# Kernel optimization log

Hardware: AMD Instinct MI355X
Metric: run time of the kernel (lower is better)

## Reference

```python
import jax, jax.numpy as jnp
import numpy as np

N, E, T, CIN, COUT = 20000, 160000, 8, 64, 128


def setup_inputs() -> dict:
    key = jax.random.key(0)
    ks = jax.random.split(key, 8)
    x = jax.random.normal(ks[0], (T, N, CIN), jnp.float32)
    edge_index = jax.random.randint(ks[1], (2, E), 0, N)
    edge_weight = jax.random.normal(ks[2], (E,), jnp.float32)
    # temporal Conv1d: kernel 3, xavier-ish small init (gain=0.1 in source)
    tconv_w = jax.random.normal(ks[3], (COUT, CIN, 3), jnp.float32) * 0.02
    tconv_b = jnp.zeros((COUT,), jnp.float32)
    ln_g = jnp.ones((COUT,), jnp.float32)
    ln_b = jnp.zeros((COUT,), jnp.float32)
    # residual 1x1 Conv1d (in != out channels)
    res_w = jax.random.normal(ks[4], (COUT, CIN), jnp.float32) * 0.05
    res_b = jnp.zeros((COUT,), jnp.float32)
    # GCNConv linear weight [out, in] and bias
    gcn_w = jax.random.normal(ks[5], (COUT, COUT), jnp.float32) * 0.05
    gcn_b = jnp.zeros((COUT,), jnp.float32)
    return dict(x=x, edge_index=edge_index, edge_weight=edge_weight,
                tconv_w=tconv_w, tconv_b=tconv_b, ln_g=ln_g, ln_b=ln_b,
                res_w=res_w, res_b=res_b, gcn_w=gcn_w, gcn_b=gcn_b)


def reference(x, edge_index, edge_weight, tconv_w, tconv_b, ln_g, ln_b,
              res_w, res_b, gcn_w, gcn_b):
    Tn, Nn, _ = x.shape
    xc = jnp.transpose(x, (1, 2, 0))  # [N, Cin, T]
    # temporal conv over T (kernel 3, pad 1)
    h = jax.lax.conv_general_dilated(
        xc, tconv_w, window_strides=(1,), padding=[(1, 1)],
        dimension_numbers=('NCH', 'OIH', 'NCH')) + tconv_b[None, :, None]
    h = jnp.transpose(h, (0, 2, 1))  # [N, T, Cout]
    # LayerNorm over channel dim
    mu = h.mean(-1, keepdims=True)
    var = ((h - mu) ** 2).mean(-1, keepdims=True)
    h = (h - mu) * jax.lax.rsqrt(var + 1e-5) * ln_g + ln_b
    h = jax.nn.relu(h)
    # 1x1 residual conv: [N,Cin,T] x [Cout,Cin] -> [N,T,Cout]
    res = jnp.einsum('nct,oc->nto', xc, res_w) + res_b
    xcmb = h + res  # [N, T, Cout]
    # --- GCNConv (PyG): softmax edge weights, self-loops, sym-normalize ---
    ew = jax.nn.softmax(edge_weight)  # softmax over all edges (dim=0)
    row, col = edge_index[0], edge_index[1]
    sl = jnp.arange(Nn)
    row_f = jnp.concatenate([row, sl])
    col_f = jnp.concatenate([col, sl])
    w_f = jnp.concatenate([ew, jnp.ones((Nn,), ew.dtype)])  # self-loop weight 1
    deg = jax.ops.segment_sum(w_f, col_f, num_segments=Nn)
    dinv = jnp.where(deg > 0, jax.lax.rsqrt(jnp.maximum(deg, 1e-12)), 0.0)
    norm = dinv[row_f] * w_f * dinv[col_f]  # [E+N]
    xt = jnp.einsum('ntc,oc->nto', xcmb, gcn_w)  # linear transform, all T at once
    msg = norm[:, None, None] * xt[row_f]        # gather sources: [E+N, T, Cout]
    agg = jax.ops.segment_sum(msg, col_f, num_segments=Nn) + gcn_b
    out = jax.nn.relu(agg)  # [N, T, Cout]
    return jnp.transpose(out, (1, 0, 2))  # [T, N, Cout] == stacked per-t list
```

## Files before the change

### kernel.cpp

```cpp
#include <hip/hip_runtime.h>
#include <math.h>

#define N_NODES 20000
#define E_EDGES 160000
#define T_STEPS 8
#define C_IN    64
#define C_OUT   128

typedef __bf16 bf16x8 __attribute__((ext_vector_type(8)));
typedef float  f32x4  __attribute__((ext_vector_type(4)));
#define MFMA16(a, b, c) __builtin_amdgcn_mfma_f32_16x16x32_bf16((a), (b), (c), 0, 0, 0)

__device__ __forceinline__ unsigned short f2u(float f) {
  __bf16 b = (__bf16)f;
  return __builtin_bit_cast(unsigned short, b);
}
__device__ __forceinline__ unsigned int pack2(float lo, float hi) {
  return (unsigned int)f2u(lo) | ((unsigned int)f2u(hi) << 16);
}

__device__ __forceinline__ float wredSum(float v) {
#pragma unroll
  for (int d = 32; d > 0; d >>= 1) v += __shfl_xor(v, d, 64);
  return v;
}
__device__ __forceinline__ float wredMax(float v) {
#pragma unroll
  for (int d = 32; d > 0; d >>= 1) v = fmaxf(v, __shfl_xor(v, d, 64));
  return v;
}
__device__ __forceinline__ int wredSumI(int v) {
#pragma unroll
  for (int d = 32; d > 0; d >>= 1) v += __shfl_xor(v, d, 64);
  return v;
}
__device__ __forceinline__ float bredSum(float v, float* sm4) {
  __syncthreads();
  v = wredSum(v);
  const int lane = threadIdx.x & 63, wid = threadIdx.x >> 6;
  if (lane == 0) sm4[wid] = v;
  __syncthreads();
  return sm4[0] + sm4[1] + sm4[2] + sm4[3];
}
__device__ __forceinline__ float bredMax(float v, float* sm4) {
  __syncthreads();
  v = wredMax(v);
  const int lane = threadIdx.x & 63, wid = threadIdx.x >> 6;
  if (lane == 0) sm4[wid] = v;
  __syncthreads();
  return fmaxf(fmaxf(sm4[0], sm4[1]), fmaxf(sm4[2], sm4[3]));
}
__device__ __forceinline__ int bredSumI(int v, int* sm4) {
  __syncthreads();
  v = wredSumI(v);
  const int lane = threadIdx.x & 63, wid = threadIdx.x >> 6;
  if (lane == 0) sm4[wid] = v;
  __syncthreads();
  return sm4[0] + sm4[1] + sm4[2] + sm4[3];
}

__global__ __launch_bounds__(256) void k_esoft(const float* __restrict__ w,
                                               float* __restrict__ pm, float* __restrict__ ps) {
  __shared__ float sm4[4];
  float m = -3.4e38f, s = 0.f;
  for (int i = blockIdx.x * 256 + threadIdx.x; i < E_EDGES; i += 256 * 256) {
    const float xw = w[i];
    if (xw > m) { s = s * expf(m - xw) + 1.f; m = xw; }
    else        { s += expf(xw - m); }
  }
  const float M = bredMax(m, sm4);
  const float sp = (s > 0.f) ? s * expf(m - M) : 0.f;
  const float S = bredSum(sp, sm4);
  if (threadIdx.x == 0) { pm[blockIdx.x] = M; ps[blockIdx.x] = S; }
}

__global__ __launch_bounds__(256) void k_edge(const float* __restrict__ w, const int* __restrict__ ei,
                                              const float* __restrict__ pm, const float* __restrict__ ps,
                                              float* __restrict__ ewv, float* __restrict__ deg,
                                              int* __restrict__ cnt) {
  __shared__ float sm4[4];
  const float mloc = pm[threadIdx.x];
  const float mx   = bredMax(mloc, sm4);
  const float sp   = ps[threadIdx.x] * expf(mloc - mx);
  const float sum  = bredSum(sp, sm4);
  const int e = blockIdx.x * 256 + threadIdx.x;
  const float v = expf(w[e] - mx) / sum;
  ewv[e] = v;
  const int c = ei[E_EDGES + e];
  atomicAdd(&deg[c], v);
  atomicAdd(&cnt[c], 1);
}

__global__ __launch_bounds__(256) void k_scanA(const int* __restrict__ cnt, const float* __restrict__ deg,
                                               float* __restrict__ dinv, int* __restrict__ csum) {
  __shared__ int sm4[4];
  const int i = blockIdx.x * 256 + threadIdx.x;
  const int v = (i < N_NODES) ? cnt[i] : 0;
  if (i < N_NODES) dinv[i] = rsqrtf(deg[i]);
  int s = wredSumI(v);
  const int lane = threadIdx.x & 63, wid = threadIdx.x >> 6;
  if (lane == 0) sm4[wid] = s;
  __syncthreads();
  if (threadIdx.x == 0) csum[blockIdx.x] = sm4[0] + sm4[1] + sm4[2] + sm4[3];
}

__global__ __launch_bounds__(256) void k_scanC(const int* __restrict__ cnt, const int* __restrict__ csum,
                                               int* __restrict__ off, int* __restrict__ cursor) {
  __shared__ int smI[4];
  __shared__ int wpart[4];
  const int tid = threadIdx.x, lane = tid & 63, wid = tid >> 6;
  const int nchunk = (N_NODES + 255) / 256;
  const int vb = (tid < nchunk && tid < blockIdx.x) ? csum[tid] : 0;
  const int base = bredSumI(vb, smI);
  const int i = blockIdx.x * 256 + tid;
  const int v = (i < N_NODES) ? cnt[i] : 0;
  int s = v;
#pragma unroll
  for (int d = 1; d < 64; d <<= 1) { const int u = __shfl_up(s, d, 64); if (lane >= d) s += u; }
  if (lane == 63) wpart[wid] = s;
  __syncthreads();
  int add = base;
#pragma unroll
  for (int wv = 0; wv < 4; ++wv) if (wv < wid) add += wpart[wv];
  if (i < N_NODES) { const int excl = add + (s - v); off[i] = excl; cursor[i] = excl; }
  if (i == N_NODES - 1) off[N_NODES] = E_EDGES;
}

__global__ __launch_bounds__(256) void k_norm_scatter(const int* __restrict__ ei, const float* __restrict__ ewv,
                                                      const float* __restrict__ dinv, int* __restrict__ cursor,
                                                      uint2* __restrict__ srcnrm) {
  const int e = blockIdx.x * 256 + threadIdx.x;
  const int r = ei[e], c = ei[E_EDGES + e];
  const float nm = dinv[r] * ewv[e] * dinv[c];
  const int pos = atomicAdd(&cursor[c], 1);
  srcnrm[pos] = make_uint2((unsigned int)r, __builtin_bit_cast(unsigned int, nm));
}

__global__ __launch_bounds__(256) void k_wprep(const float* __restrict__ tconv_w, const float* __restrict__ res_w,
                                               const float* __restrict__ gcn_w, unsigned int* __restrict__ Bf,
                                               float* __restrict__ deg, int* __restrict__ cnt) {
  const int gid = blockIdx.x * 256 + threadIdx.x;
  if (gid < N_NODES) { deg[gid] = 1.0f; cnt[gid] = 0; }
  float v0, v1;
  if (gid < 12288) {
    const int reg = gid & 3, l = (gid >> 2) & 63, ct = (gid >> 8) & 7, ks = gid >> 11;
    const int o = ct * 16 + (l & 15);
    const int k0 = ks * 32 + ((l >> 4) & 3) * 8 + reg * 2;
    const int c0 = k0 & 63, tap0 = k0 >> 6;
    const int c1 = (k0 + 1) & 63, tap1 = (k0 + 1) >> 6;
    v0 = tconv_w[o * 192 + c0 * 3 + tap0];
    v1 = tconv_w[o * 192 + c1 * 3 + tap1];
  } else if (gid < 16384) {
    const int g = gid - 12288;
    const int reg = g & 3, l = (g >> 2) & 63, ct = (g >> 8) & 7, ks = g >> 11;
    const int o = ct * 16 + (l & 15);
    const int k0 = ks * 32 + ((l >> 4) & 3) * 8 + reg * 2;
    v0 = res_w[o * 64 + k0];
    v1 = res_w[o * 64 + k0 + 1];
  } else {
    const int g = gid - 16384;
    const int reg = g & 3, l = (g >> 2) & 63, ct = (g >> 8) & 7, ks = g >> 11;
    const int o = ct * 16 + (l & 15);
    const int k0 = ks * 32 + ((l >> 4) & 3) * 8 + reg * 2;
    v0 = gcn_w[o * 128 + k0];
    v1 = gcn_w[o * 128 + k0 + 1];
  }
  Bf[gid] = pack2(v0, v1);
}

#define XS_NODE 720
#define XS_SLOT 72
#define AS2_STRIDE 136
__global__ __launch_bounds__(256, 2) void k_fuse(const float* __restrict__ x,
                                                 const float* __restrict__ tconv_b,
                                                 const float* __restrict__ ln_g, const float* __restrict__ ln_b,
                                                 const float* __restrict__ res_b,
                                                 const unsigned int* __restrict__ Bf,
                                                 unsigned char* __restrict__ xq,
                                                 float* __restrict__ qsc) {
  const int tid = threadIdx.x, lane = tid & 63, w = tid >> 6;
  const int l15 = lane & 15, lg = lane >> 4;
  const int n0 = blockIdx.x * 16;

  __shared__ __align__(16) unsigned short XsAs[128 * AS2_STRIDE];
  unsigned short* Xs  = XsAs;
  unsigned short* As2 = XsAs;
  __shared__ float psum[4][128], psq[4][128];
  __shared__ float smu[128], srs[128];
  __shared__ float pmax4[4][16];
  __shared__ float smax16[16];

#pragma unroll
  for (int p = 0; p < 8; ++p) {
    const int chunk = p * 256 + tid;
    const int tq = chunk >> 8, nn = (chunk >> 4) & 15, c4 = chunk & 15;
    const float4 v = *(const float4*)(x + ((size_t)tq * N_NODES + n0 + nn) * C_IN + c4 * 4);
    uint2 pk; pk.x = pack2(v.x, v.y); pk.y = pack2(v.z, v.w);
    *(uint2*)&Xs[nn * XS_NODE + (tq + 1) * XS_SLOT + c4 * 4] = pk;
  }
#pragma unroll
  for (int p = 0; p < 3; ++p) {
    const int i = p * 256 + tid;
    if (i < 576) {
      const int nn = i / 36;
      const int r = i - nn * 36;
      const int sl = (r < 18) ? 0 : 9;
      const int of = ((r < 18) ? r : r - 18) * 4;
      *(uint2*)&Xs[nn * XS_NODE + sl * XS_SLOT + of] = make_uint2(0u, 0u);
    }
  }

  const uint4* Bf4 = (const uint4*)Bf;
  uint4 Bc[2][6], Br[2][2];
#pragma unroll
  for (int ct = 0; ct < 2; ++ct) {
    const int ctg = w * 2 + ct;
#pragma unroll
    for (int ks = 0; ks < 6; ++ks) Bc[ct][ks] = Bf4[(ks * 8 + ctg) * 64 + lane];
#pragma unroll
    for (int ks = 0; ks < 2; ++ks) Br[ct][ks] = Bf4[3072 + (ks * 8 + ctg) * 64 + lane];
  }
  float cb[2], rb[2], gv[2], bv[2];
#pragma unroll
  for (int ct = 0; ct < 2; ++ct) {
    const int col = w * 32 + ct * 16 + l15;
    cb[ct] = tconv_b[col]; rb[ct] = res_b[col]; gv[ct] = ln_g[col]; bv[ct] = ln_b[col];
  }
  __syncthreads();

  f32x4 accC[8][2], accR[8][2];
#pragma unroll
  for (int rt = 0; rt < 8; ++rt)
#pragma unroll
    for (int ct = 0; ct < 2; ++ct) { accC[rt][ct] = (f32x4)0.f; accR[rt][ct] = (f32x4)0.f; }

#pragma unroll
  for (int ks = 0; ks < 6; ++ks) {
    bf16x8 af[8];
    const int slot = (l15 & 7) + (ks >> 1);
    const int koff = slot * XS_SLOT + (ks & 1) * 32 + lg * 8;
#pragma unroll
    for (int rt = 0; rt < 8; ++rt) {
      const int node = rt * 2 + (l15 >> 3);
      af[rt] = *(const bf16x8*)&Xs[node * XS_NODE + koff];
    }
#pragma unroll
    for (int rt = 0; rt < 8; ++rt)
#pragma unroll
      for (int ct = 0; ct < 2; ++ct)
        accC[rt][ct] = MFMA16(af[rt], __builtin_bit_cast(bf16x8, Bc[ct][ks]), accC[rt][ct]);
    if (ks == 2 || ks == 3) {
#pragma unroll
      for (int rt = 0; rt < 8; ++rt)
#pragma unroll
        for (int ct = 0; ct < 2; ++ct)
          accR[rt][ct] = MFMA16(af[rt], __builtin_bit_cast(bf16x8, Br[ct][ks - 2]), accR[rt][ct]);
    }
  }

#pragma unroll
  for (int rt = 0; rt < 8; ++rt) {
    float s[4], s2[4];
#pragma unroll
    for (int j = 0; j < 4; ++j) {
      const float h0 = accC[rt][0][j] + cb[0];
      const float h1 = accC[rt][1][j] + cb[1];
      accC[rt][0][j] = h0; accC[rt][1][j] = h1;
      s[j] = h0 + h1; s2[j] = h0 * h0 + h1 * h1;
    }
#pragma unroll
    for (int d = 1; d < 16; d <<= 1)
#pragma unroll
      for (int j = 0; j < 4; ++j) { s[j] += __shfl_xor(s[j], d, 64); s2[j] += __shfl_xor(s2[j], d, 64); }
    if (l15 == 0)
#pragma unroll
      for (int j = 0; j < 4; ++j) {
        psum[w][rt * 16 + lg * 4 + j] = s[j];
        psq[w][rt * 16 + lg * 4 + j] = s2[j];
      }
  }
  __syncthreads();
  if (tid < 128) {
    const float S  = psum[0][tid] + psum[1][tid] + psum[2][tid] + psum[3][tid];
    const float S2 = psq[0][tid] + psq[1][tid] + psq[2][tid] + psq[3][tid];
    const float mu = S * (1.f / 128.f);
    const float var = S2 * (1.f / 128.f) - mu * mu;
    smu[tid] = mu; srs[tid] = rsqrtf(var + 1e-5f);
  }
  __syncthreads();

#pragma unroll
  for (int rt = 0; rt < 8; ++rt)
#pragma unroll
    for (int j = 0; j < 4; ++j) {
      const int row = rt * 16 + lg * 4 + j;
      const float mu = smu[row], rs = srs[row];
      const int sw = ((row >> 3) & 1) << 4;
#pragma unroll
      for (int ct = 0; ct < 2; ++ct) {
        float xc = (accC[rt][ct][j] - mu) * rs * gv[ct] + bv[ct];
        xc = fmaxf(xc, 0.f) + accR[rt][ct][j] + rb[ct];
        const int col = w * 32 + ct * 16 + l15;
        As2[row * AS2_STRIDE + (col ^ sw)] = f2u(xc);
      }
    }
  __syncthreads();

  uint4 Bg[2][4];
#pragma unroll
  for (int ct = 0; ct < 2; ++ct)
#pragma unroll
    for (int ks = 0; ks < 4; ++ks) Bg[ct][ks] = Bf4[4096 + (ks * 8 + (w * 2 + ct)) * 64 + lane];

  f32x4 acc[8][2];
#pragma unroll
  for (int rt = 0; rt < 8; ++rt)
#pragma unroll
    for (int ct = 0; ct < 2; ++ct) acc[rt][ct] = (f32x4)0.f;

  const int swr = ((l15 >> 3) & 1) << 4;
#pragma unroll
  for (int ks = 0; ks < 4; ++ks) {
    bf16x8 af[8];
    const int koff = (ks * 32 + lg * 8) ^ swr;
#pragma unroll
    for (int rt = 0; rt < 8; ++rt)
      af[rt] = *(const bf16x8*)&As2[(rt * 16 + l15) * AS2_STRIDE + koff];
#pragma unroll
    for (int rt = 0; rt < 8; ++rt)
#pragma unroll
      for (int ct = 0; ct < 2; ++ct)
        acc[rt][ct] = MFMA16(af[rt], __builtin_bit_cast(bf16x8, Bg[ct][ks]), acc[rt][ct]);
  }

#pragma unroll
  for (int rt = 0; rt < 8; ++rt) {
    float m = 0.f;
#pragma unroll
    for (int ct = 0; ct < 2; ++ct)
#pragma unroll
      for (int j = 0; j < 4; ++j) m = fmaxf(m, fabsf(acc[rt][ct][j]));
#pragma unroll
    for (int d = 1; d < 32; d <<= 1) m = fmaxf(m, __shfl_xor(m, d, 64));
    if ((lane & 31) == 0) pmax4[w][rt * 2 + (lane >> 5)] = m;
  }
  __syncthreads();
  if (tid < 16) {
    const float mx = fmaxf(fmaxf(pmax4[0][tid], pmax4[1][tid]), fmaxf(pmax4[2][tid], pmax4[3][tid]));
    smax16[tid] = mx;
    qsc[n0 + tid] = mx * (1.f / 127.f);
  }
  __syncthreads();

  const int t0 = (lg & 1) * 4;
#pragma unroll
  for (int rt = 0; rt < 8; ++rt) {
    const int nn = rt * 2 + (lg >> 1);
    const size_t n = (size_t)(n0 + nn);
    const float mx = smax16[nn];
    const float inv = (mx > 0.f) ? 127.f / mx : 0.f;
#pragma unroll
    for (int ct = 0; ct < 2; ++ct) {
      const int col = w * 32 + ct * 16 + l15;
      unsigned int pk8 = 0;
#pragma unroll
      for (int j = 0; j < 4; ++j) {
        const int q = (int)rintf(acc[rt][ct][j] * inv) + 128;
        pk8 |= ((unsigned int)q) << (8 * j);
      }
      *(unsigned int*)(xq + (n * C_OUT + col) * T_STEPS + t0) = pk8;
    }
  }
}

__global__ __launch_bounds__(256) void k_agg(const unsigned char* __restrict__ xq,
                                             const float* __restrict__ qsc,
                                             const uint2* __restrict__ srcnrm,
                                             const int* __restrict__ off, const float* __restrict__ dinv,
                                             const float* __restrict__ gcn_b, float* __restrict__ out) {
  const int tid = threadIdx.x, lane = tid & 63, w = tid >> 6;
  const int j = blockIdx.x * 4 + w;
  const int s = off[j], e = off[j + 1];
  const float d2 = dinv[j] * dinv[j];

  float acc[2][8];
#pragma unroll
  for (int h = 0; h < 2; ++h)
#pragma unroll
    for (int t = 0; t < 8; ++t) acc[h][t] = 0.f;

  float summul;
  {
    const float mul = d2 * qsc[j];
    summul = mul;
    const uint2 qa = *(const uint2*)(xq + ((size_t)j * C_OUT + lane) * T_STEPS);
    const uint2 qb = *(const uint2*)(xq + ((size_t)j * C_OUT + 64 + lane) * T_STEPS);
#pragma unroll
    for (int tt = 0; tt < 4; ++tt) {
      acc[0][tt]     = fmaf((float)((qa.x >> (8 * tt)) & 0xffu), mul, acc[0][tt]);
      acc[0][4 + tt] = fmaf((float)((qa.y >> (8 * tt)) & 0xffu), mul, acc[0][4 + tt]);
      acc[1][tt]     = fmaf((float)((qb.x >> (8 * tt)) & 0xffu), mul, acc[1][tt]);
      acc[1][4 + tt] = fmaf((float)((qb.y >> (8 * tt)) & 0xffu), mul, acc[1][4 + tt]);
    }
  }

  for (int k = s; k < e; ++k) {
    const uint2 sn = srcnrm[k];
    const int r = (int)sn.x;
    const float mul = __builtin_bit_cast(float, sn.y) * qsc[r];
    summul += mul;
    const uint2 qa = *(const uint2*)(xq + ((size_t)r * C_OUT + lane) * T_STEPS);
    const uint2 qb = *(const uint2*)(xq + ((size_t)r * C_OUT + 64 + lane) * T_STEPS);
#pragma unroll
    for (int tt = 0; tt < 4; ++tt) {
      acc[0][tt]     = fmaf((float)((qa.x >> (8 * tt)) & 0xffu), mul, acc[0][tt]);
      acc[0][4 + tt] = fmaf((float)((qa.y >> (8 * tt)) & 0xffu), mul, acc[0][4 + tt]);
      acc[1][tt]     = fmaf((float)((qb.x >> (8 * tt)) & 0xffu), mul, acc[1][tt]);
      acc[1][4 + tt] = fmaf((float)((qb.y >> (8 * tt)) & 0xffu), mul, acc[1][4 + tt]);
    }
  }

  const float corr = 128.f * summul;
  const float b0 = gcn_b[lane], b1 = gcn_b[64 + lane];
#pragma unroll
  for (int h = 0; h < 2; ++h) {
    const float bo = h ? b1 : b0;
#pragma unroll
    for (int t = 0; t < 8; ++t) {
      const float v = acc[h][t] - corr + bo;
      out[((size_t)t * N_NODES + j) * C_OUT + h * 64 + lane] = fmaxf(v, 0.f);
    }
  }
}

extern "C" void kernel_launch(void* const* d_in, const int* in_sizes, int n_in,
                              void* d_out, int out_size, void* d_ws, size_t ws_size,
                              hipStream_t stream) {
  (void)in_sizes; (void)n_in; (void)out_size; (void)ws_size;
  const float* x       = (const float*)d_in[0];
  const int*   ei      = (const int*)d_in[1];
  const float* ewt     = (const float*)d_in[2];
  const float* tconv_w = (const float*)d_in[3];
  const float* tconv_b = (const float*)d_in[4];
  const float* ln_g    = (const float*)d_in[5];
  const float* ln_b    = (const float*)d_in[6];
  const float* res_w   = (const float*)d_in[7];
  const float* res_b   = (const float*)d_in[8];
  const float* gcn_w   = (const float*)d_in[9];
  const float* gcn_b   = (const float*)d_in[10];
  float* out = (float*)d_out;

  unsigned char* xq = (unsigned char*)d_ws;
  float* qsc  = (float*)(xq + (size_t)N_NODES * C_OUT * T_STEPS);
  unsigned int* Bf = (unsigned int*)(qsc + N_NODES);
  float* ewv   = (float*)(Bf + 24576);
  float* deg   = ewv + E_EDGES;
  float* dinv  = deg + N_NODES;
  float* pm    = dinv + N_NODES;
  float* ps    = pm + 256;
  int*   cnt    = (int*)(ps + 256);
  int*   off    = cnt + N_NODES;
  int*   cursor = off + N_NODES + 1;
  int*   csum   = cursor + N_NODES;
  uint2* srcnrm = (uint2*)(((size_t)(csum + 128) + 15) & ~(size_t)15);

  const int nblk = (N_NODES + 255) / 256;
  const int eblk = E_EDGES / 256;

  k_wprep<<<96, 256, 0, stream>>>(tconv_w, res_w, gcn_w, Bf, deg, cnt);
  k_esoft<<<256, 256, 0, stream>>>(ewt, pm, ps);
  k_edge<<<eblk, 256, 0, stream>>>(ewt, ei, pm, ps, ewv, deg, cnt);
  k_scanA<<<nblk, 256, 0, stream>>>(cnt, deg, dinv, csum);
  k_scanC<<<nblk, 256, 0, stream>>>(cnt, csum, off, cursor);
  k_norm_scatter<<<eblk, 256, 0, stream>>>(ei, ewv, dinv, cursor, srcnrm);

  k_fuse<<<1250, 256, 0, stream>>>(x, tconv_b, ln_g, ln_b, res_b, Bf, xq, qsc);
  k_agg<<<N_NODES / 4, 256, 0, stream>>>(xq, qsc, srcnrm, off, dinv, gcn_b, out);
}
```

Measured before the change: 133.3 us.

## Fuse graph preprocessing kernels into one cooperative kernel with grid syncs

The six small preprocessing kernels (weight prep, edge softmax partials, edge normalize/degree, two scan passes, CSR scatter) are merged into a single cooperative kernel of 625 blocks, separated by grid.sync barriers. This removes five kernel launch boundaries and their drain/launch gaps. The softmax partial reduction now uses one element per thread and a 625-entry second-level merge, so the pm/ps workspace grows. Grid-wide barriers add their own cost, and the launch relies on all 625 blocks being co-resident.

```diff
diff --git a/kernel.cpp b/kernel.cpp
--- a/kernel.cpp
+++ b/kernel.cpp
@@ -1,5 +1,8 @@
 #include <hip/hip_runtime.h>
+#include <hip/hip_cooperative_groups.h>
 #include <math.h>
+
+namespace cg = cooperative_groups;
 
 #define N_NODES 20000
 #define E_EDGES 160000
@@ -59,113 +62,113 @@
   return sm4[0] + sm4[1] + sm4[2] + sm4[3];
 }
 
-__global__ __launch_bounds__(256) void k_esoft(const float* __restrict__ w,
-                                               float* __restrict__ pm, float* __restrict__ ps) {
+__global__ __launch_bounds__(256) void k_graph(const float* __restrict__ tconv_w, const float* __restrict__ res_w,
+                                               const float* __restrict__ gcn_w, const float* __restrict__ ewt,
+                                               const int* __restrict__ ei,
+                                               unsigned int* __restrict__ Bf,
+                                               float* __restrict__ deg, int* __restrict__ cnt,
+                                               float* __restrict__ dinv, float* __restrict__ ewv,
+                                               float* __restrict__ pm, float* __restrict__ ps,
+                                               int* __restrict__ off, int* __restrict__ cursor,
+                                               int* __restrict__ csum, uint2* __restrict__ srcnrm) {
+  cg::grid_group grid = cg::this_grid();
   __shared__ float sm4[4];
-  float m = -3.4e38f, s = 0.f;
-  for (int i = blockIdx.x * 256 + threadIdx.x; i < E_EDGES; i += 256 * 256) {
-    const float xw = w[i];
-    if (xw > m) { s = s * expf(m - xw) + 1.f; m = xw; }
-    else        { s += expf(xw - m); }
-  }
-  const float M = bredMax(m, sm4);
-  const float sp = (s > 0.f) ? s * expf(m - M) : 0.f;
-  const float S = bredSum(sp, sm4);
-  if (threadIdx.x == 0) { pm[blockIdx.x] = M; ps[blockIdx.x] = S; }
-}
-
-__global__ __launch_bounds__(256) void k_edge(const float* __restrict__ w, const int* __restrict__ ei,
-                                              const float* __restrict__ pm, const float* __restrict__ ps,
-                                              float* __restrict__ ewv, float* __restrict__ deg,
-                                              int* __restrict__ cnt) {
-  __shared__ float sm4[4];
-  const float mloc = pm[threadIdx.x];
-  const float mx   = bredMax(mloc, sm4);
-  const float sp   = ps[threadIdx.x] * expf(mloc - mx);
-  const float sum  = bredSum(sp, sm4);
-  const int e = blockIdx.x * 256 + threadIdx.x;
-  const float v = expf(w[e] - mx) / sum;
-  ewv[e] = v;
-  const int c = ei[E_EDGES + e];
-  atomicAdd(&deg[c], v);
-  atomicAdd(&cnt[c], 1);
-}
-
-__global__ __launch_bounds__(256) void k_scanA(const int* __restrict__ cnt, const float* __restrict__ deg,
-                                               float* __restrict__ dinv, int* __restrict__ csum) {
-  __shared__ int sm4[4];
-  const int i = blockIdx.x * 256 + threadIdx.x;
-  const int v = (i < N_NODES) ? cnt[i] : 0;
-  if (i < N_NODES) dinv[i] = rsqrtf(deg[i]);
-  int s = wredSumI(v);
-  const int lane = threadIdx.x & 63, wid = threadIdx.x >> 6;
-  if (lane == 0) sm4[wid] = s;
-  __syncthreads();
-  if (threadIdx.x == 0) csum[blockIdx.x] = sm4[0] + sm4[1] + sm4[2] + sm4[3];
-}
-
-__global__ __launch_bounds__(256) void k_scanC(const int* __restrict__ cnt, const int* __restrict__ csum,
-                                               int* __restrict__ off, int* __restrict__ cursor) {
   __shared__ int smI[4];
   __shared__ int wpart[4];
-  const int tid = threadIdx.x, lane = tid & 63, wid = tid >> 6;
-  const int nchunk = (N_NODES + 255) / 256;
-  const int vb = (tid < nchunk && tid < blockIdx.x) ? csum[tid] : 0;
-  const int base = bredSumI(vb, smI);
-  const int i = blockIdx.x * 256 + tid;
-  const int v = (i < N_NODES) ? cnt[i] : 0;
-  int s = v;
-#pragma unroll
-  for (int d = 1; d < 64; d <<= 1) { const int u = __shfl_up(s, d, 64); if (lane >= d) s += u; }
-  if (lane == 63) wpart[wid] = s;
-  __syncthreads();
-  int add = base;
-#pragma unroll
-  for (int wv = 0; wv < 4; ++wv) if (wv < wid) add += wpart[wv];
-  if (i < N_NODES) { const int excl = add + (s - v); off[i] = excl; cursor[i] = excl; }
-  if (i == N_NODES - 1) off[N_NODES] = E_EDGES;
-}
-
-__global__ __launch_bounds__(256) void k_norm_scatter(const int* __restrict__ ei, const float* __restrict__ ewv,
-                                                      const float* __restrict__ dinv, int* __restrict__ cursor,
-                                                      uint2* __restrict__ srcnrm) {
-  const int e = blockIdx.x * 256 + threadIdx.x;
-  const int r = ei[e], c = ei[E_EDGES + e];
-  const float nm = dinv[r] * ewv[e] * dinv[c];
-  const int pos = atomicAdd(&cursor[c], 1);
-  srcnrm[pos] = make_uint2((unsigned int)r, __builtin_bit_cast(unsigned int, nm));
-}
-
-__global__ __launch_bounds__(256) void k_wprep(const float* __restrict__ tconv_w, const float* __restrict__ res_w,
-                                               const float* __restrict__ gcn_w, unsigned int* __restrict__ Bf,
-                                               float* __restrict__ deg, int* __restrict__ cnt) {
-  const int gid = blockIdx.x * 256 + threadIdx.x;
+  const int tid = threadIdx.x, bid = blockIdx.x;
+  const int gid = bid * 256 + tid;
+  const int lane = tid & 63, wid = tid >> 6;
+
   if (gid < N_NODES) { deg[gid] = 1.0f; cnt[gid] = 0; }
-  float v0, v1;
-  if (gid < 12288) {
-    const int reg = gid & 3, l = (gid >> 2) & 63, ct = (gid >> 8) & 7, ks = gid >> 11;
-    const int o = ct * 16 + (l & 15);
-    const int k0 = ks * 32 + ((l >> 4) & 3) * 8 + reg * 2;
-    const int c0 = k0 & 63, tap0 = k0 >> 6;
-    const int c1 = (k0 + 1) & 63, tap1 = (k0 + 1) >> 6;
-    v0 = tconv_w[o * 192 + c0 * 3 + tap0];
-    v1 = tconv_w[o * 192 + c1 * 3 + tap1];
-  } else if (gid < 16384) {
-    const int g = gid - 12288;
-    const int reg = g & 3, l = (g >> 2) & 63, ct = (g >> 8) & 7, ks = g >> 11;
-    const int o = ct * 16 + (l & 15);
-    const int k0 = ks * 32 + ((l >> 4) & 3) * 8 + reg * 2;
-    v0 = res_w[o * 64 + k0];
-    v1 = res_w[o * 64 + k0 + 1];
-  } else {
-    const int g = gid - 16384;
-    const int reg = g & 3, l = (g >> 2) & 63, ct = (g >> 8) & 7, ks = g >> 11;
-    const int o = ct * 16 + (l & 15);
-    const int k0 = ks * 32 + ((l >> 4) & 3) * 8 + reg * 2;
-    v0 = gcn_w[o * 128 + k0];
-    v1 = gcn_w[o * 128 + k0 + 1];
-  }
-  Bf[gid] = pack2(v0, v1);
+  if (gid < 24576) {
+    float v0, v1;
+    if (gid < 12288) {
+      const int reg = gid & 3, l = (gid >> 2) & 63, ct = (gid >> 8) & 7, ks = gid >> 11;
+      const int o = ct * 16 + (l & 15);
+      const int k0 = ks * 32 + ((l >> 4) & 3) * 8 + reg * 2;
+      const int c0 = k0 & 63, tap0 = k0 >> 6;
+      const int c1 = (k0 + 1) & 63, tap1 = (k0 + 1) >> 6;
+      v0 = tconv_w[o * 192 + c0 * 3 + tap0];
+      v1 = tconv_w[o * 192 + c1 * 3 + tap1];
+    } else if (gid < 16384) {
+      const int g = gid - 12288;
+      const int reg = g & 3, l = (g >> 2) & 63, ct = (g >> 8) & 7, ks = g >> 11;
+      const int o = ct * 16 + (l & 15);
+      const int k0 = ks * 32 + ((l >> 4) & 3) * 8 + reg * 2;
+      v0 = res_w[o * 64 + k0];
+      v1 = res_w[o * 64 + k0 + 1];
+    } else {
+      const int g = gid - 16384;
+      const int reg = g & 3, l = (g >> 2) & 63, ct = (g >> 8) & 7, ks = g >> 11;
+      const int o = ct * 16 + (l & 15);
+      const int k0 = ks * 32 + ((l >> 4) & 3) * 8 + reg * 2;
+      v0 = gcn_w[o * 128 + k0];
+      v1 = gcn_w[o * 128 + k0 + 1];
+    }
+    Bf[gid] = pack2(v0, v1);
+  }
+  const float we = ewt[gid];
+  {
+    const float M = bredMax(we, sm4);
+    const float S = bredSum(expf(we - M), sm4);
+    if (tid == 0) { pm[bid] = M; ps[bid] = S; }
+  }
+  grid.sync();
+
+  {
+    float m = -3.4e38f, s = 0.f;
+    for (int t = tid; t < 625; t += 256) {
+      const float mi = pm[t], si = ps[t];
+      if (mi > m) { s = s * expf(m - mi) + si; m = mi; }
+      else        { s += si * expf(mi - m); }
+    }
+    const float M = bredMax(m, sm4);
+    const float sp = s * expf(m - M);
+    const float S = bredSum(sp, sm4);
+    const float v = expf(we - M) / S;
+    ewv[gid] = v;
+    const int c = ei[E_EDGES + gid];
+    atomicAdd(&deg[c], v);
+    atomicAdd(&cnt[c], 1);
+  }
+  grid.sync();
+
+  if (bid < 79) {
+    const int i = gid;
+    const int v = (i < N_NODES) ? cnt[i] : 0;
+    if (i < N_NODES) dinv[i] = rsqrtf(deg[i]);
+    int s = wredSumI(v);
+    __syncthreads();
+    if (lane == 0) smI[wid] = s;
+    __syncthreads();
+    if (tid == 0) csum[bid] = smI[0] + smI[1] + smI[2] + smI[3];
+  }
+  grid.sync();
+
+  if (bid < 79) {
+    const int vb = (tid < 79 && tid < bid) ? csum[tid] : 0;
+    const int base = bredSumI(vb, smI);
+    const int i = gid;
+    const int v = (i < N_NODES) ? cnt[i] : 0;
+    int s = v;
+#pragma unroll
+    for (int d = 1; d < 64; d <<= 1) { const int u = __shfl_up(s, d, 64); if (lane >= d) s += u; }
+    if (lane == 63) wpart[wid] = s;
+    __syncthreads();
+    int add = base;
+#pragma unroll
+    for (int wv = 0; wv < 4; ++wv) if (wv < wid) add += wpart[wv];
+    if (i < N_NODES) { const int excl = add + (s - v); off[i] = excl; cursor[i] = excl; }
+    if (i == N_NODES - 1) off[N_NODES] = E_EDGES;
+  }
+  grid.sync();
+
+  {
+    const int r = ei[gid], c = ei[E_EDGES + gid];
+    const float nm = dinv[r] * ewv[gid] * dinv[c];
+    const int pos = atomicAdd(&cursor[c], 1);
+    srcnrm[pos] = make_uint2((unsigned int)r, __builtin_bit_cast(unsigned int, nm));
+  }
 }
 
 #define XS_NODE 720
@@ -457,22 +460,19 @@
   float* deg   = ewv + E_EDGES;
   float* dinv  = deg + N_NODES;
   float* pm    = dinv + N_NODES;
-  float* ps    = pm + 256;
-  int*   cnt    = (int*)(ps + 256);
+  float* ps    = pm + 640;
+  int*   cnt    = (int*)(ps + 640);
   int*   off    = cnt + N_NODES;
   int*   cursor = off + N_NODES + 1;
   int*   csum   = cursor + N_NODES;
   uint2* srcnrm = (uint2*)(((size_t)(csum + 128) + 15) & ~(size_t)15);
 
-  const int nblk = (N_NODES + 255) / 256;
-  const int eblk = E_EDGES / 256;
-
-  k_wprep<<<96, 256, 0, stream>>>(tconv_w, res_w, gcn_w, Bf, deg, cnt);
-  k_esoft<<<256, 256, 0, stream>>>(ewt, pm, ps);
-  k_edge<<<eblk, 256, 0, stream>>>(ewt, ei, pm, ps, ewv, deg, cnt);
-  k_scanA<<<nblk, 256, 0, stream>>>(cnt, deg, dinv, csum);
-  k_scanC<<<nblk, 256, 0, stream>>>(cnt, csum, off, cursor);
-  k_norm_scatter<<<eblk, 256, 0, stream>>>(ei, ewv, dinv, cursor, srcnrm);
+  void* args[] = {
+    (void*)&tconv_w, (void*)&res_w, (void*)&gcn_w, (void*)&ewt, (void*)&ei,
+    (void*)&Bf, (void*)&deg, (void*)&cnt, (void*)&dinv, (void*)&ewv,
+    (void*)&pm, (void*)&ps, (void*)&off, (void*)&cursor, (void*)&csum, (void*)&srcnrm,
+  };
+  hipLaunchCooperativeKernel((const void*)k_graph, dim3(E_EDGES / 256), dim3(256), args, 0, stream);
 
   k_fuse<<<1250, 256, 0, stream>>>(x, tconv_b, ln_g, ln_b, res_b, Bf, xq, qsc);
   k_agg<<<N_NODES / 4, 256, 0, stream>>>(xq, qsc, srcnrm, off, dinv, gcn_b, out);
```

Result: slower. 382.2 us (+186.7%).
